# Kernel tuning notes

Measured on AMD Instinct MI355X. Metric: run time of the kernel, lower is better.

Reference implementation:

```python
import jax, jax.numpy as jnp
import numpy as np
from jax import lax

EPS = 1e-5

def index_points(points, idx):
    # points [B,N,C], idx [B,...] int -> [B,...,C]
    return jax.vmap(lambda p, i: p[i])(points, idx)

def square_distance(a, b):
    # a [B,S,3], b [B,N,3] -> [B,S,N] squared euclidean
    return (jnp.sum(a * a, -1)[:, :, None] + jnp.sum(b * b, -1)[:, None, :]
            - 2.0 * jnp.einsum('bsc,bnc->bsn', a, b))

def farthest_point_sample(xyz, npoint):
    # deterministic FPS starting at index 0 (torch version starts at a random index)
    B, N, _ = xyz.shape
    def step(carry, _):
        dist, farthest = carry
        centroid = jax.vmap(lambda p, i: p[i])(xyz, farthest)  # [B,3]
        d = jnp.sum((xyz - centroid[:, None, :]) ** 2, -1)     # [B,N]
        dist = jnp.minimum(dist, d)
        nxt = jnp.argmax(dist, -1).astype(jnp.int32)
        return (dist, nxt), farthest
    init = (jnp.full((B, N), 1e10, xyz.dtype), jnp.zeros((B,), jnp.int32))
    _, idx = lax.scan(step, init, None, length=npoint)
    return jnp.transpose(idx)  # [B, npoint]

def ball_query(radius, nsample, xyz, new_xyz):
    # replicate the torch arange/mask/sort trick: first nsample in-index-order points within radius
    B, N, _ = xyz.shape
    S = new_xyz.shape[1]
    sqrdists = square_distance(new_xyz, xyz)                      # [B,S,N]
    idx = jnp.broadcast_to(jnp.arange(N, dtype=jnp.int32), (B, S, N))
    idx = jnp.where(sqrdists > radius * radius, N, idx)
    idx = jnp.sort(idx, axis=-1)[:, :, :nsample]                  # [B,S,K]
    first = idx[:, :, :1]
    return jnp.where(idx == N, first, idx)

def conv_bn_relu(x, W, b, gamma, beta):
    # 1x1 Conv2d == per-point linear; BatchNorm2d (training mode) over (B, S, K) per channel
    h = jnp.einsum('bskc,oc->bsko', x, W) + b
    mean = jnp.mean(h, axis=(0, 1, 2))
    var = jnp.var(h, axis=(0, 1, 2))
    h = (h - mean) * (gamma / jnp.sqrt(var + EPS)) + beta
    return jax.nn.relu(h)

def set_abstraction(xyz, points, npoint, radius, nsample, W, b, gamma, beta):
    fps_idx = farthest_point_sample(xyz, npoint)                  # [B,S]
    new_xyz = index_points(xyz, fps_idx)                          # [B,S,3]
    idx = ball_query(radius, nsample, xyz, new_xyz)               # [B,S,K]
    grouped_xyz = index_points(xyz, idx) - new_xyz[:, :, None, :] # [B,S,K,3]
    if points is not None:
        new_points = jnp.concatenate([grouped_xyz, index_points(points, idx)], -1)
    else:
        new_points = grouped_xyz
    h = conv_bn_relu(new_points, W, b, gamma, beta)
    return new_xyz, jnp.max(h, axis=2)                            # [B,S,Cout]

def set_abstraction_all(xyz, points, W, b, gamma, beta):
    grouped = jnp.concatenate([xyz, points], -1)[:, None]         # [B,1,N,3+C]
    h = conv_bn_relu(grouped, W, b, gamma, beta)
    return jnp.max(h, axis=2)[:, 0]                               # [B,Cout]


def setup_inputs() -> dict:
    key = jax.random.key(0)
    ks = jax.random.split(key, 6)
    B, N, Z = 8, 8192, 256
    def lin(k, o, i):
        return jax.random.normal(k, (o, i), jnp.float32) * (1.0 / np.sqrt(i))
    f32 = jnp.float32
    return {
        'xyz': jax.random.uniform(ks[0], (B, N, 3), f32),
        'w1': lin(ks[1], 128, 3),   'b1': jnp.zeros((128,), f32),
        'g1': jnp.ones((128,), f32), 'be1': jnp.zeros((128,), f32),
        'w2': lin(ks[2], 256, 131), 'b2': jnp.zeros((256,), f32),
        'g2': jnp.ones((256,), f32), 'be2': jnp.zeros((256,), f32),
        'w3': lin(ks[3], 512, 259), 'b3': jnp.zeros((512,), f32),
        'g3': jnp.ones((512,), f32), 'be3': jnp.zeros((512,), f32),
        'wf': lin(ks[4], Z, 512),   'bf': jnp.zeros((Z,), f32),
    }


def reference(xyz, w1, b1, g1, be1, w2, b2, g2, be2, w3, b3, g3, be3, wf, bf):
    # PointNet2Encoder.forward (normal_channel=False): three set-abstraction layers + fc
    l1_xyz, l1_pts = set_abstraction(xyz, None, 512, 0.2, 32, w1, b1, g1, be1)
    l2_xyz, l2_pts = set_abstraction(l1_xyz, l1_pts, 128, 0.4, 64, w2, b2, g2, be2)
    l3 = set_abstraction_all(l2_xyz, l2_pts, w3, b3, g3, be3)     # [B,512]
    return l3 @ wf.T + bf                                         # [B, z_dim]
```

## Files before the change

kernel.cpp:

```cpp
#include <hip/hip_runtime.h>
#include <hip/hip_bf16.h>
#include <cstddef>
#include <cstdint>


__device__ __forceinline__ void fma16(float* acc, float4 a, float4 b) {
  acc[0]  = fmaf(a.x, b.x, acc[0]);
  acc[1]  = fmaf(a.x, b.y, acc[1]);
  acc[2]  = fmaf(a.x, b.z, acc[2]);
  acc[3]  = fmaf(a.x, b.w, acc[3]);
  acc[4]  = fmaf(a.y, b.x, acc[4]);
  acc[5]  = fmaf(a.y, b.y, acc[5]);
  acc[6]  = fmaf(a.y, b.z, acc[6]);
  acc[7]  = fmaf(a.y, b.w, acc[7]);
  acc[8]  = fmaf(a.z, b.x, acc[8]);
  acc[9]  = fmaf(a.z, b.y, acc[9]);
  acc[10] = fmaf(a.z, b.z, acc[10]);
  acc[11] = fmaf(a.z, b.w, acc[11]);
  acc[12] = fmaf(a.w, b.x, acc[12]);
  acc[13] = fmaf(a.w, b.y, acc[13]);
  acc[14] = fmaf(a.w, b.z, acc[14]);
  acc[15] = fmaf(a.w, b.w, acc[15]);
}

#define DPP_FMAX(v, ctrl)                                                     \
  (v) = fmaxf((v), __int_as_float(__builtin_amdgcn_update_dpp(                \
                 0, __float_as_int(v), (ctrl), 0xf, 0xf, true)))

__device__ __forceinline__ float wave_max_dpp(float v) {
  DPP_FMAX(v, 0x111);
  DPP_FMAX(v, 0x112);
  DPP_FMAX(v, 0x114);
  DPP_FMAX(v, 0x118);
  DPP_FMAX(v, 0x142);
  DPP_FMAX(v, 0x143);
  return __int_as_float(__builtin_amdgcn_readlane(__float_as_int(v), 63));
}

__device__ __forceinline__ float readlane_f(float v, int l) {
  return __int_as_float(__builtin_amdgcn_readlane(__float_as_int(v), l));
}

template<int N, int NPOINT, int TPB>
__launch_bounds__(TPB)
__global__ void fps_kernel(const float* __restrict__ xyz,
                           int* __restrict__ out_idx,
                           float* __restrict__ out_xyz) {
  constexpr int PPT = N / TPB;
  constexpr int NW = TPB / 64;
  static_assert(NW == 8, "cross-wave DPP reduce assumes 8 waves");
  __shared__ float s_wval[NW];
  __shared__ __align__(16) float4 s_hist[NPOINT];
  const int b = blockIdx.x;
  const int t = threadIdx.x;
  const int lane = t & 63;
  const int wid = t >> 6;
  const float* xb = xyz + (size_t)b * N * 3;
  float px[PPT], py[PPT], pz[PPT], dist[PPT];
#pragma unroll
  for (int j = 0; j < PPT; ++j) {
    const int n = t * PPT + j;
    px[j] = xb[n * 3 + 0];
    py[j] = xb[n * 3 + 1];
    pz[j] = xb[n * 3 + 2];
    dist[j] = 1e10f;
  }
  float cx = xb[0], cy = xb[1], cz = xb[2];
  if (t == 0) s_hist[0] = make_float4(__int_as_float(0), cx, cy, cz);
  for (int i = 0; i < NPOINT - 1; ++i) {
    float m = -1.0f;
#pragma unroll
    for (int j = 0; j < PPT; ++j) {
      const float dx = __fsub_rn(px[j], cx);
      const float dy = __fsub_rn(py[j], cy);
      const float dz = __fsub_rn(pz[j], cz);
      const float d = __fadd_rn(__fadd_rn(__fmul_rn(dx, dx), __fmul_rn(dy, dy)),
                                __fmul_rn(dz, dz));
      const float nd = fminf(dist[j], d);
      dist[j] = nd;
      m = fmaxf(m, nd);
    }
    const float wv = wave_max_dpp(m);
    if (lane == 0) s_wval[wid] = wv;
    __syncthreads();
    float x = s_wval[lane & 7];
    float y = x;
    DPP_FMAX(y, 0x111);
    DPP_FMAX(y, 0x112);
    DPP_FMAX(y, 0x114);
    const float winner =
        __int_as_float(__builtin_amdgcn_readlane(__float_as_int(y), 7));
    const unsigned long long wmask = __ballot(x == winner);
    const int first_w = __ffsll(wmask) - 1;
    if (wid == first_w) {
      const unsigned long long cand = __ballot(m == winner);
      const int fl = __ffsll(cand) - 1;
      if (lane == fl) {
        int fj = 0;
        float fx = px[0], fy = py[0], fz = pz[0];
        bool found = (dist[0] == winner);
#pragma unroll
        for (int j = 1; j < PPT; ++j) {
          const bool hit = !found && (dist[j] == winner);
          if (hit) { fj = j; fx = px[j]; fy = py[j]; fz = pz[j]; found = true; }
        }
        s_hist[i + 1] = make_float4(__int_as_float(t * PPT + fj), fx, fy, fz);
      }
    }
    __syncthreads();
    const float4 pk = s_hist[i + 1];
    cx = pk.y; cy = pk.z; cz = pk.w;
  }
  for (int e = t; e < NPOINT; e += TPB) {
    const float4 h = s_hist[e];
    out_idx[b * NPOINT + e] = __float_as_int(h.x);
    float* o = out_xyz + ((size_t)b * NPOINT + e) * 3;
    o[0] = h.y; o[1] = h.z; o[2] = h.w;
  }
}

template<int N, int NPOINT>
__launch_bounds__(64)
__global__ void wave_fps_kernel(const float* __restrict__ xyz,
                                int* __restrict__ out_idx,
                                float* __restrict__ out_xyz) {
  constexpr int PPT = N / 64;
  const int b = blockIdx.x;
  const int lane = threadIdx.x;
  const float* xb = xyz + (size_t)b * N * 3;
  float px[PPT], py[PPT], pz[PPT], dist[PPT];
#pragma unroll
  for (int j = 0; j < PPT; ++j) {
    const int n = lane * PPT + j;
    px[j] = xb[n * 3 + 0];
    py[j] = xb[n * 3 + 1];
    pz[j] = xb[n * 3 + 2];
    dist[j] = 1e10f;
  }
  int far = 0;
  float cx = xb[0], cy = xb[1], cz = xb[2];
  for (int i = 0; i < NPOINT; ++i) {
    if (lane == 0) {
      out_idx[b * NPOINT + i] = far;
      float* o = out_xyz + ((size_t)b * NPOINT + i) * 3;
      o[0] = cx; o[1] = cy; o[2] = cz;
    }
    float m = -1.0f;
    int mj = 0;
    float mx = px[0], my = py[0], mz = pz[0];
#pragma unroll
    for (int j = 0; j < PPT; ++j) {
      const float dx = __fsub_rn(px[j], cx);
      const float dy = __fsub_rn(py[j], cy);
      const float dz = __fsub_rn(pz[j], cz);
      const float d = __fadd_rn(__fadd_rn(__fmul_rn(dx, dx), __fmul_rn(dy, dy)),
                                __fmul_rn(dz, dz));
      const float nd = fminf(dist[j], d);
      dist[j] = nd;
      const bool better = nd > m;
      m = better ? nd : m;
      mj = better ? j : mj;
      mx = better ? px[j] : mx;
      my = better ? py[j] : my;
      mz = better ? pz[j] : mz;
    }
    const float wv = wave_max_dpp(m);
    const unsigned long long cand = __ballot(m == wv);
    const int fl = __ffsll(cand) - 1;
    far = __builtin_amdgcn_readlane(lane * PPT + mj, fl);
    cx = readlane_f(mx, fl);
    cy = readlane_f(my, fl);
    cz = readlane_f(mz, fl);
  }
}

template<int N, int S, int NS>
__global__ void ballq_kernel(const float* __restrict__ xyz,
                             const float* __restrict__ new_xyz,
                             int* __restrict__ out_idx,
                             float r2) {
  const int gw = (blockIdx.x * blockDim.x + threadIdx.x) >> 6;
  const int lane = threadIdx.x & 63;
  if (gw >= 8 * S) return;
  const int b = gw / S;
  const int s = gw % S;
  const float* c = new_xyz + ((size_t)b * S + s) * 3;
  const float cx = c[0], cy = c[1], cz = c[2];
  const float sa = __fadd_rn(__fadd_rn(__fmul_rn(cx, cx), __fmul_rn(cy, cy)),
                             __fmul_rn(cz, cz));
  const float* xb = xyz + (size_t)b * N * 3;
  int* out = out_idx + ((size_t)b * S + s) * NS;
  int cnt = 0;
  int first = -1;
  for (int n0 = 0; n0 < N && cnt < NS; n0 += 64) {
    const int n = n0 + lane;
    const float x = xb[n * 3 + 0];
    const float y = xb[n * 3 + 1];
    const float z = xb[n * 3 + 2];
    const float sb = __fadd_rn(__fadd_rn(__fmul_rn(x, x), __fmul_rn(y, y)),
                               __fmul_rn(z, z));
    const float dt = __fadd_rn(__fadd_rn(__fmul_rn(x, cx), __fmul_rn(y, cy)),
                               __fmul_rn(z, cz));
    const float d = __fsub_rn(__fadd_rn(sa, sb), __fmul_rn(2.0f, dt));
    const bool in = !(d > r2);
    const unsigned long long m = __ballot(in);
    if (in) {
      const int pos = cnt + __popcll(m & ((1ull << lane) - 1ull));
      if (pos < NS) out[pos] = n;
    }
    if (first < 0 && m) first = n0 + __ffsll((unsigned long long)m) - 1;
    cnt += __popcll(m);
  }
  for (int j = cnt + lane; j < NS; j += 64) out[j] = first;
}

__global__ void mom1_kernel(const float* __restrict__ xyz,
                            const float* __restrict__ l1_xyz,
                            const int* __restrict__ idx1,
                            float* __restrict__ part) {
  const int t = threadIdx.x;
  const int r = blockIdx.x * 256 + t;
  const int bs = r >> 5;
  const int b = r >> 14;
  const int idx = idx1[r];
  const float* p = xyz + ((size_t)(b << 13) + idx) * 3;
  const float* q = l1_xyz + (size_t)bs * 3;
  const float x = p[0] - q[0];
  const float y = p[1] - q[1];
  const float z = p[2] - q[2];
  float vals[9] = {x, y, z, x * x, x * y, x * z, y * y, y * z, z * z};
  __shared__ float sw[4][9];
  const int lane = t & 63, wid = t >> 6;
#pragma unroll
  for (int v = 0; v < 9; ++v) {
    float a = vals[v];
#pragma unroll
    for (int off = 32; off; off >>= 1) a += __shfl_xor(a, off);
    if (lane == 0) sw[wid][v] = a;
  }
  __syncthreads();
  if (t == 0) {
#pragma unroll
    for (int v = 0; v < 9; ++v)
      part[blockIdx.x * 12 + v] = sw[0][v] + sw[1][v] + sw[2][v] + sw[3][v];
  }
}

__global__ void stats1_kernel(const float* __restrict__ part,
                              const float* __restrict__ w1,
                              const float* __restrict__ b1,
                              const float* __restrict__ g1,
                              const float* __restrict__ be1,
                              float* __restrict__ ss1) {
  __shared__ double sm[9];
  const int t = threadIdx.x;
  if (t < 9) {
    double a = 0.0;
    for (int k = 0; k < 512; ++k) a += (double)part[k * 12 + t];
    sm[t] = a;
  }
  __syncthreads();
  const double n = 131072.0;
  const double mu0 = sm[0] / n, mu1 = sm[1] / n, mu2 = sm[2] / n;
  const double C00 = sm[3] / n - mu0 * mu0;
  const double C01 = sm[4] / n - mu0 * mu1;
  const double C02 = sm[5] / n - mu0 * mu2;
  const double C11 = sm[6] / n - mu1 * mu1;
  const double C12 = sm[7] / n - mu1 * mu2;
  const double C22 = sm[8] / n - mu2 * mu2;
  if (t < 128) {
    const double w0 = w1[t * 3], w1_ = w1[t * 3 + 1], w2 = w1[t * 3 + 2];
    const double mh = w0 * mu0 + w1_ * mu1 + w2 * mu2 + (double)b1[t];
    const double var = w0 * w0 * C00 + w1_ * w1_ * C11 + w2 * w2 * C22 +
                       2.0 * (w0 * w1_ * C01 + w0 * w2 * C02 + w1_ * w2 * C12);
    const float scale = g1[t] / sqrtf((float)var + 1e-5f);
    const float shift = be1[t] - (float)mh * scale;
    ss1[t * 2] = scale;
    ss1[t * 2 + 1] = shift;
  }
}

__global__ void conv1max_kernel(const float* __restrict__ xyz,
                                const float* __restrict__ l1_xyz,
                                const int* __restrict__ idx1,
                                const float* __restrict__ w1,
                                const float* __restrict__ b1,
                                const float* __restrict__ ss1,
                                float* __restrict__ l1_pts) {
  const int bs = blockIdx.x;
  const int b = bs >> 9;
  const int t = threadIdx.x;
  __shared__ float sx[32][3];
  if (t < 32) {
    const int idx = idx1[bs * 32 + t];
    const float* p = xyz + ((size_t)(b << 13) + idx) * 3;
    const float* q = l1_xyz + (size_t)bs * 3;
    sx[t][0] = p[0] - q[0];
    sx[t][1] = p[1] - q[1];
    sx[t][2] = p[2] - q[2];
  }
  __syncthreads();
  const float w0 = w1[t * 3], wa = w1[t * 3 + 1], wb = w1[t * 3 + 2];
  const float bo = b1[t];
  float hmax = -1e30f, hmin = 1e30f;
#pragma unroll 8
  for (int k = 0; k < 32; ++k) {
    const float h = sx[k][0] * w0 + sx[k][1] * wa + sx[k][2] * wb + bo;
    hmax = fmaxf(hmax, h);
    hmin = fminf(hmin, h);
  }
  const float scale = ss1[t * 2], shift = ss1[t * 2 + 1];
  const float hsel = (scale >= 0.f) ? hmax : hmin;
  l1_pts[(size_t)bs * 128 + t] = fmaxf(hsel * scale + shift, 0.0f);
}

#define MOM2_BLOCKS 256
#define MOM2_S2 (132 * 132)
#define MOM2_STRIDE (MOM2_S2 + 132)

__global__ __launch_bounds__(256)
void mom2_kernel(const float* __restrict__ l1_xyz,
                 const float* __restrict__ l1_pts,
                 const float* __restrict__ l2_xyz,
                 const int* __restrict__ idx2,
                 float* __restrict__ part) {
  __shared__ __align__(16) float xs[64 * 136];
  const int t = threadIdx.x;
  const int blk = blockIdx.x;
  int ti = -1, tj = 0;
  {
    int u = t;
    for (int r = 0; r < 17; ++r) {
      const int cnt = 17 - r;
      if (u < cnt) { ti = r; tj = r + u; break; }
      u -= cnt;
    }
  }
  const bool active = (ti >= 0);
  float acc[64];
#pragma unroll
  for (int j = 0; j < 64; ++j) acc[j] = 0.f;
  float s1 = 0.f;
  const int rbase = blk * 256;
  for (int sb = 0; sb < 4; ++sb) {
    __syncthreads();
    for (int e = t; e < 64 * 136; e += 256) {
      const int rr = e / 136, cc = e % 136;
      const int r = rbase + sb * 64 + rr;
      const int b = r >> 13;
      const int s = (r >> 6) & 127;
      const int idx = idx2[r];
      float v = 0.f;
      if (cc < 3)
        v = l1_xyz[((size_t)(b << 9) + idx) * 3 + cc] -
            l2_xyz[((size_t)(b << 7) + s) * 3 + cc];
      else if (cc < 131)
        v = l1_pts[((size_t)(b << 9) + idx) * 128 + (cc - 3)];
      xs[rr * 136 + cc] = v;
    }
    __syncthreads();
    if (active) {
      for (int r = 0; r < 64; ++r) {
        const float4 a0 = *(const float4*)&xs[r * 136 + ti * 8];
        const float4 a1 = *(const float4*)&xs[r * 136 + ti * 8 + 4];
        const float4 b0 = *(const float4*)&xs[r * 136 + tj * 8];
        const float4 b1 = *(const float4*)&xs[r * 136 + tj * 8 + 4];
        fma16(acc + 0,  a0, b0);
        fma16(acc + 16, a0, b1);
        fma16(acc + 32, a1, b0);
        fma16(acc + 48, a1, b1);
      }
    }
    if (t < 132) {
      for (int r = 0; r < 64; ++r) s1 += xs[r * 136 + t];
    }
  }
  float* pb = part + (size_t)blk * MOM2_STRIDE;
  if (active) {
#pragma unroll
    for (int ii = 0; ii < 8; ++ii) {
      const int gi = ti * 8 + ii;
      if (gi < 132) {
#pragma unroll
        for (int jj = 0; jj < 8; ++jj) {
          const int gj = tj * 8 + jj;
          if (gj < 132) {
            const float v =
                acc[(ii >> 2) * 32 + (jj >> 2) * 16 + (ii & 3) * 4 + (jj & 3)];
            pb[gi * 132 + gj] = v;
            if (ti != tj) pb[gj * 132 + gi] = v;
          }
        }
      }
    }
  }
  if (t < 132) pb[MOM2_S2 + t] = s1;
}

__global__ void reduce2_kernel(const float* __restrict__ part,
                               double* __restrict__ out) {
  const int e = blockIdx.x * 256 + threadIdx.x;
  if (e >= MOM2_STRIDE) return;
  double a = 0.0;
  for (int k = 0; k < MOM2_BLOCKS; ++k)
    a += (double)part[(size_t)k * MOM2_STRIDE + e];
  out[e] = a;
}

__global__ void stats2_kernel(const double* __restrict__ mom,
                              const float* __restrict__ w2,
                              const float* __restrict__ b2,
                              const float* __restrict__ g2,
                              const float* __restrict__ be2,
                              float* __restrict__ ss2) {
  const int o = blockIdx.x;
  const int t = threadIdx.x;
  const float* w = w2 + o * 131;
  double q = 0.0, md = 0.0;
  for (int i = t; i < 131; i += 128) {
    const double wi = (double)w[i];
    double di = 0.0;
    for (int j = 0; j < 131; ++j) di += mom[i * 132 + j] * (double)w[j];
    q += wi * di;
    md += wi * mom[MOM2_S2 + i];
  }
  __shared__ double sq[128], smd[128];
  sq[t] = q;
  smd[t] = md;
  __syncthreads();
  for (int off = 64; off; off >>= 1) {
    if (t < off) { sq[t] += sq[t + off]; smd[t] += smd[t + off]; }
    __syncthreads();
  }
  if (t == 0) {
    const double n = 65536.0;
    const double mdot = smd[0] / n;
    const double var = sq[0] / n - mdot * mdot;
    const double mean = mdot + (double)b2[o];
    const float scale = g2[o] / sqrtf((float)var + 1e-5f);
    const float shift = be2[o] - (float)mean * scale;
    ss2[o * 2] = scale;
    ss2[o * 2 + 1] = shift;
  }
}

__global__ __launch_bounds__(256)
void conv2max_kernel(const float* __restrict__ l1_xyz,
                     const float* __restrict__ l1_pts,
                     const float* __restrict__ l2_xyz,
                     const int* __restrict__ idx2,
                     const float* __restrict__ w2,
                     const float* __restrict__ b2,
                     const float* __restrict__ ss2,
                     float* __restrict__ l2_pts) {
  __shared__ __align__(16) float xT[33 * 68];
  __shared__ __align__(16) float wT[33 * 260];
  __shared__ float redmax[8 * 256];
  __shared__ float redmin[8 * 256];
  const int bs = blockIdx.x;
  const int b = bs >> 7;
  const int t = threadIdx.x;
  const int ty = t >> 5;
  const int tx = t & 31;
  float acc[64];
#pragma unroll
  for (int j = 0; j < 64; ++j) acc[j] = 0.f;
  for (int ch = 0; ch < 4; ++ch) {
    const int c0 = ch * 33;
    const int CC = (ch == 3) ? 32 : 33;
    __syncthreads();
    for (int e = t; e < 64 * CC; e += 256) {
      const int k = e / CC, cc = e % CC;
      const int idx = idx2[bs * 64 + k];
      const int c = c0 + cc;
      float v;
      if (c < 3)
        v = l1_xyz[((size_t)(b << 9) + idx) * 3 + c] -
            l2_xyz[(size_t)bs * 3 + c];
      else
        v = l1_pts[((size_t)(b << 9) + idx) * 128 + (c - 3)];
      xT[cc * 68 + k] = v;
    }
    for (int e = t; e < 256 * CC; e += 256) {
      const int oo = e / CC, cc = e % CC;
      wT[cc * 260 + oo] = w2[oo * 131 + c0 + cc];
    }
    __syncthreads();
    for (int cc = 0; cc < CC; ++cc) {
      const float4 a0 = *(const float4*)&xT[cc * 68 + ty * 8];
      const float4 a1 = *(const float4*)&xT[cc * 68 + ty * 8 + 4];
      const float4 w0 = *(const float4*)&wT[cc * 260 + tx * 4];
      const float4 w1 = *(const float4*)&wT[cc * 260 + 128 + tx * 4];
      fma16(acc + 0,  a0, w0);
      fma16(acc + 16, a0, w1);
      fma16(acc + 32, a1, w0);
      fma16(acc + 48, a1, w1);
    }
  }
#pragma unroll
  for (int bi = 0; bi < 4; ++bi) {
    float mxA = acc[bi], mnA = acc[bi];
    float mxB = acc[16 + bi], mnB = acc[16 + bi];
#pragma unroll
    for (int ai = 1; ai < 4; ++ai) {
      mxA = fmaxf(mxA, acc[ai * 4 + bi]);
      mnA = fminf(mnA, acc[ai * 4 + bi]);
      mxB = fmaxf(mxB, acc[16 + ai * 4 + bi]);
      mnB = fminf(mnB, acc[16 + ai * 4 + bi]);
    }
#pragma unroll
    for (int ai = 0; ai < 4; ++ai) {
      mxA = fmaxf(mxA, acc[32 + ai * 4 + bi]);
      mnA = fminf(mnA, acc[32 + ai * 4 + bi]);
      mxB = fmaxf(mxB, acc[48 + ai * 4 + bi]);
      mnB = fminf(mnB, acc[48 + ai * 4 + bi]);
    }
    redmax[ty * 256 + tx * 4 + bi] = mxA;
    redmin[ty * 256 + tx * 4 + bi] = mnA;
    redmax[ty * 256 + 128 + tx * 4 + bi] = mxB;
    redmin[ty * 256 + 128 + tx * 4 + bi] = mnB;
  }
  __syncthreads();
  {
    const int o = t;
    float mx = redmax[o], mn = redmin[o];
#pragma unroll
    for (int w = 1; w < 8; ++w) {
      mx = fmaxf(mx, redmax[w * 256 + o]);
      mn = fminf(mn, redmin[w * 256 + o]);
    }
    const float bo = b2[o];
    const float hmax = mx + bo;
    const float hmin = mn + bo;
    const float scale = ss2[o * 2], shift = ss2[o * 2 + 1];
    const float hsel = (scale >= 0.f) ? hmax : hmin;
    l2_pts[(size_t)bs * 256 + o] = fmaxf(hsel * scale + shift, 0.f);
  }
}

__global__ __launch_bounds__(256)
void conv3_kernel(const float* __restrict__ l2_xyz,
                  const float* __restrict__ l2_pts,
                  const float* __restrict__ w3,
                  const float* __restrict__ b3,
                  float* __restrict__ h3T) {
  __shared__ __align__(16) float aT[96 * 68];
  __shared__ __align__(16) float wT[96 * 68];
  const int t = threadIdx.x;
  const int r0 = (blockIdx.x & 15) * 64;
  const int o0 = (blockIdx.x >> 4) * 64;
  const int ty = t >> 4, tx = t & 15;
  float acc[16];
#pragma unroll
  for (int j = 0; j < 16; ++j) acc[j] = 0.f;
  for (int c0 = 0; c0 < 259; c0 += 96) {
    __syncthreads();
    for (int e = t; e < 96 * 64; e += 256) {
      const int rr = e / 96, cc = e - rr * 96;
      const int c = c0 + cc;
      const int r = r0 + rr;
      float v = 0.f;
      if (c < 259)
        v = (c < 3) ? l2_xyz[(size_t)r * 3 + c]
                    : l2_pts[(size_t)r * 256 + (c - 3)];
      aT[cc * 68 + rr] = v;
    }
    for (int e = t; e < 96 * 64; e += 256) {
      const int oo = e / 96, cc = e - oo * 96;
      const int c = c0 + cc;
      wT[cc * 68 + oo] = (c < 259) ? w3[(size_t)(o0 + oo) * 259 + c] : 0.f;
    }
    __syncthreads();
    for (int cc = 0; cc < 96; ++cc) {
      const float4 a = *(const float4*)&aT[cc * 68 + ty * 4];
      const float4 w4 = *(const float4*)&wT[cc * 68 + tx * 4];
      fma16(acc, a, w4);
    }
  }
#pragma unroll
  for (int kk = 0; kk < 4; ++kk)
#pragma unroll
    for (int oo = 0; oo < 4; ++oo) {
      const int o = o0 + tx * 4 + oo;
      const int r = r0 + ty * 4 + kk;
      h3T[(size_t)o * 1024 + r] = acc[kk * 4 + oo] + b3[o];
    }
}

__global__ void bn3max_kernel(const float* __restrict__ h3T,
                              const float* __restrict__ g3,
                              const float* __restrict__ be3,
                              float* __restrict__ l3) {
  const int o = blockIdx.x;
  const int t = threadIdx.x;
  const float4 v = *(const float4*)&h3T[(size_t)o * 1024 + t * 4];
  double s = (double)v.x + (double)v.y + (double)v.z + (double)v.w;
  double s2 = (double)v.x * v.x + (double)v.y * v.y + (double)v.z * v.z +
              (double)v.w * v.w;
  __shared__ double sa_[256], sb_[256];
  sa_[t] = s;
  sb_[t] = s2;
  __syncthreads();
  for (int off = 128; off; off >>= 1) {
    if (t < off) { sa_[t] += sa_[t + off]; sb_[t] += sb_[t + off]; }
    __syncthreads();
  }
  const double mean = sa_[0] / 1024.0;
  const double var = sb_[0] / 1024.0 - mean * mean;
  const float scale = g3[o] / sqrtf((float)var + 1e-5f);
  const float shift = be3[o] - (float)mean * scale;
  const float hmax = fmaxf(fmaxf(v.x, v.y), fmaxf(v.z, v.w));
  const float hmin = fminf(fminf(v.x, v.y), fminf(v.z, v.w));
  const float hsel = (scale >= 0.f) ? hmax : hmin;
  __shared__ float rm[256];
  rm[t] = fmaxf(hsel * scale + shift, 0.f);
  __syncthreads();
  if (t < 8) {
    float m = rm[t * 32];
#pragma unroll
    for (int j = 1; j < 32; ++j) m = fmaxf(m, rm[t * 32 + j]);
    l3[t * 512 + o] = m;
  }
}

__global__ void final_kernel(const float* __restrict__ l3,
                             const float* __restrict__ wf,
                             const float* __restrict__ bf,
                             float* __restrict__ out) {
  const int b = blockIdx.x;
  const int t = threadIdx.x;
  __shared__ float s[512];
  s[t] = l3[b * 512 + t];
  s[t + 256] = l3[b * 512 + t + 256];
  __syncthreads();
  float acc = bf[t];
  for (int o = 0; o < 512; ++o) acc = fmaf(wf[(size_t)t * 512 + o], s[o], acc);
  out[b * 256 + t] = acc;
}

extern "C" void kernel_launch(void* const* d_in, const int* in_sizes, int n_in,
                              void* d_out, int out_size, void* d_ws, size_t ws_size,
                              hipStream_t stream) {
  (void)in_sizes; (void)n_in; (void)out_size; (void)ws_size;
  const float* xyz = (const float*)d_in[0];
  const float* w1 = (const float*)d_in[1];
  const float* b1 = (const float*)d_in[2];
  const float* g1 = (const float*)d_in[3];
  const float* be1 = (const float*)d_in[4];
  const float* w2 = (const float*)d_in[5];
  const float* b2 = (const float*)d_in[6];
  const float* g2 = (const float*)d_in[7];
  const float* be2 = (const float*)d_in[8];
  const float* w3 = (const float*)d_in[9];
  const float* b3 = (const float*)d_in[10];
  const float* g3 = (const float*)d_in[11];
  const float* be3 = (const float*)d_in[12];
  const float* wf = (const float*)d_in[13];
  const float* bf = (const float*)d_in[14];
  float* out = (float*)d_out;

  char* base = (char*)d_ws;
  size_t off = 0;
  auto alloc = [&](size_t bytes) -> char* {
    off = (off + 511) & ~(size_t)511;
    char* p = base + off;
    off += bytes;
    return p;
  };
  int* fps1_idx = (int*)alloc(8 * 512 * 4);
  float* l1_xyz = (float*)alloc(8 * 512 * 3 * 4);
  int* idx1 = (int*)alloc((size_t)8 * 512 * 32 * 4);
  float* part1 = (float*)alloc(512 * 12 * 4);
  float* ss1 = (float*)alloc(128 * 2 * 4);
  float* l1_pts = (float*)alloc((size_t)8 * 512 * 128 * 4);
  int* fps2_idx = (int*)alloc(8 * 128 * 4);
  float* l2_xyz = (float*)alloc(8 * 128 * 3 * 4);
  int* idx2 = (int*)alloc((size_t)8 * 128 * 64 * 4);
  float* part2 = (float*)alloc((size_t)MOM2_BLOCKS * MOM2_STRIDE * 4);
  double* mom2d = (double*)alloc((size_t)MOM2_STRIDE * 8);
  float* ss2 = (float*)alloc(256 * 2 * 4);
  float* l2_pts = (float*)alloc((size_t)8 * 128 * 256 * 4);
  float* h3T = (float*)alloc((size_t)512 * 1024 * 4);
  float* l3 = (float*)alloc(8 * 512 * 4);

  const float r2_1 = (float)(0.2 * 0.2);
  const float r2_2 = (float)(0.4 * 0.4);

  fps_kernel<8192, 512, 512><<<8, 512, 0, stream>>>(xyz, fps1_idx, l1_xyz);
  ballq_kernel<8192, 512, 32><<<1024, 256, 0, stream>>>(xyz, l1_xyz, idx1, r2_1);
  mom1_kernel<<<512, 256, 0, stream>>>(xyz, l1_xyz, idx1, part1);
  stats1_kernel<<<1, 128, 0, stream>>>(part1, w1, b1, g1, be1, ss1);
  conv1max_kernel<<<4096, 128, 0, stream>>>(xyz, l1_xyz, idx1, w1, b1, ss1, l1_pts);
  wave_fps_kernel<512, 128><<<8, 64, 0, stream>>>(l1_xyz, fps2_idx, l2_xyz);
  ballq_kernel<512, 128, 64><<<256, 256, 0, stream>>>(l1_xyz, l2_xyz, idx2, r2_2);
  mom2_kernel<<<MOM2_BLOCKS, 256, 0, stream>>>(l1_xyz, l1_pts, l2_xyz, idx2, part2);
  reduce2_kernel<<<(MOM2_STRIDE + 255) / 256, 256, 0, stream>>>(part2, mom2d);
  stats2_kernel<<<256, 128, 0, stream>>>(mom2d, w2, b2, g2, be2, ss2);
  conv2max_kernel<<<1024, 256, 0, stream>>>(l1_xyz, l1_pts, l2_xyz, idx2, w2, b2,
                                            ss2, l2_pts);
  conv3_kernel<<<128, 256, 0, stream>>>(l2_xyz, l2_pts, w3, b3, h3T);
  bn3max_kernel<<<512, 256, 0, stream>>>(h3T, g3, be3, l3);
  final_kernel<<<8, 256, 0, stream>>>(l3, wf, bf, out);
}
```

Before: 1.123 ms.

## Cut FPS iteration to one barrier via per-wave candidate publishing

Each wave now finds its own argmax lane and writes a candidate (value, coordinates, index) to double-buffered shared memory before a single barrier. Every thread then reduces the eight candidates and reads the winning coordinates directly, so the second barrier and the serialized winner lookup are gone. The cost is that all waves do the local argmax search every iteration, plus some extra LDS traffic. Double buffering on the iteration parity prevents a write-after-read race between iterations.

Measured after the change: 1.207 ms. 1.07x slower.

```diff
diff --git a/kernel.cpp b/kernel.cpp
--- a/kernel.cpp
+++ b/kernel.cpp
@@ -49,7 +49,8 @@
   constexpr int PPT = N / TPB;
   constexpr int NW = TPB / 64;
   static_assert(NW == 8, "cross-wave DPP reduce assumes 8 waves");
-  __shared__ float s_wval[NW];
+  __shared__ __align__(16) float4 s_cand[2][NW];
+  __shared__ int s_cidx[2][NW];
   __shared__ __align__(16) float4 s_hist[NPOINT];
   const int b = blockIdx.x;
   const int t = threadIdx.x;
@@ -81,36 +82,38 @@
       m = fmaxf(m, nd);
     }
     const float wv = wave_max_dpp(m);
-    if (lane == 0) s_wval[wid] = wv;
-    __syncthreads();
-    float x = s_wval[lane & 7];
-    float y = x;
+    const unsigned long long cand = __ballot(m == wv);
+    const int fl = __ffsll(cand) - 1;
+    const int p = i & 1;
+    if (lane == fl) {
+      int fj = 0;
+      float fx = px[0], fy = py[0], fz = pz[0];
+      bool found = (dist[0] == wv);
+#pragma unroll
+      for (int j = 1; j < PPT; ++j) {
+        const bool hit = !found && (dist[j] == wv);
+        if (hit) { fj = j; fx = px[j]; fy = py[j]; fz = pz[j]; found = true; }
+      }
+      s_cand[p][wid] = make_float4(wv, fx, fy, fz);
+      s_cidx[p][wid] = t * PPT + fj;
+    }
+    __syncthreads();
+    const float4 c4 = s_cand[p][lane & 7];
+    float y = c4.x;
     DPP_FMAX(y, 0x111);
     DPP_FMAX(y, 0x112);
     DPP_FMAX(y, 0x114);
-    const float winner =
-        __int_as_float(__builtin_amdgcn_readlane(__float_as_int(y), 7));
-    const unsigned long long wmask = __ballot(x == winner);
-    const int first_w = __ffsll(wmask) - 1;
-    if (wid == first_w) {
-      const unsigned long long cand = __ballot(m == winner);
-      const int fl = __ffsll(cand) - 1;
-      if (lane == fl) {
-        int fj = 0;
-        float fx = px[0], fy = py[0], fz = pz[0];
-        bool found = (dist[0] == winner);
-#pragma unroll
-        for (int j = 1; j < PPT; ++j) {
-          const bool hit = !found && (dist[j] == winner);
-          if (hit) { fj = j; fx = px[j]; fy = py[j]; fz = pz[j]; found = true; }
-        }
-        s_hist[i + 1] = make_float4(__int_as_float(t * PPT + fj), fx, fy, fz);
-      }
-    }
-    __syncthreads();
-    const float4 pk = s_hist[i + 1];
-    cx = pk.y; cy = pk.z; cz = pk.w;
-  }
+    const float winner = readlane_f(y, 7);
+    const unsigned long long wmask = __ballot(c4.x == winner);
+    const int wstar = __ffsll(wmask) - 1;
+    cx = readlane_f(c4.y, wstar);
+    cy = readlane_f(c4.z, wstar);
+    cz = readlane_f(c4.w, wstar);
+    if (t == 0)
+      s_hist[i + 1] =
+          make_float4(__int_as_float(s_cidx[p][wstar]), cx, cy, cz);
+  }
+  __syncthreads();
   for (int e = t; e < NPOINT; e += TPB) {
     const float4 h = s_hist[e];
     out_idx[b * NPOINT + e] = __float_as_int(h.x);
```
